# Kernel tuning notes

Hardware: AMD Instinct MI355X
Metric: run time of the kernel (lower is better)

## Reference

```python
import jax, jax.numpy as jnp
import numpy as np

N_NODES = 50000
N_EDGES = 800000
D = 64
IN_DIM = 100
N_GRAPHS = 512
N_LAYERS = 3
OUT_DIM = 24  # n_lbs * n_tasks
BN_EPS = 1e-5


def setup_inputs() -> dict:
    key = jax.random.key(0)
    ks = iter(jax.random.split(key, 40))

    def w(shape):
        fan_in = shape[0]
        return jax.random.normal(next(ks), shape, jnp.float32) / np.float32(np.sqrt(fan_in))

    inp = {}
    inp["x"] = jax.random.normal(next(ks), (N_NODES, IN_DIM), jnp.float32)
    inp["edge_index"] = jax.random.randint(next(ks), (2, N_EDGES), 0, N_NODES, jnp.int32)
    inp["batch"] = jnp.sort(jax.random.randint(next(ks), (N_NODES,), 0, N_GRAPHS, jnp.int32))

    dims_in = [IN_DIM, D, D]
    for i in range(N_LAYERS):
        inp[f"w1_{i}"] = w((dims_in[i], D))
        inp[f"b1_{i}"] = jnp.zeros((D,), jnp.float32)
        inp[f"w2_{i}"] = w((D, D))
        inp[f"b2_{i}"] = jnp.zeros((D,), jnp.float32)

    inp["jk_w"] = w((N_LAYERS * D, D))
    inp["jk_b"] = jnp.zeros((D,), jnp.float32)
    inp["ffn_w1"] = w((D, D))
    inp["ffn_b1"] = jnp.zeros((D,), jnp.float32)
    inp["bn_g"] = jnp.ones((D,), jnp.float32)
    inp["bn_b"] = jnp.zeros((D,), jnp.float32)
    inp["bn_m"] = 0.1 * jax.random.normal(next(ks), (D,), jnp.float32)
    inp["bn_v"] = jax.random.uniform(next(ks), (D,), jnp.float32, 0.5, 1.5)
    inp["ffn_w2"] = w((D, D))
    inp["ffn_b2"] = jnp.zeros((D,), jnp.float32)
    inp["out_w"] = w((D, OUT_DIM))
    inp["out_b"] = jnp.zeros((OUT_DIM,), jnp.float32)
    return inp


def _gin_conv(h, src, dst, w1, b1, w2, b2):
    # sum-aggregate neighbor messages:  agg[dst] += h[src]
    agg = jax.ops.segment_sum(h[src], dst, num_segments=N_NODES)
    z = h + agg  # eps = 0 -> (1 + eps) * x + agg
    # GINConv internal MLP: lin -> relu -> lin (no norm, plain last)
    return jnp.maximum(z @ w1 + b1, 0.0) @ w2 + b2


def reference(x, edge_index, batch,
              w1_0, b1_0, w2_0, b2_0,
              w1_1, b1_1, w2_1, b2_1,
              w1_2, b1_2, w2_2, b2_2,
              jk_w, jk_b,
              ffn_w1, ffn_b1, bn_g, bn_b, bn_m, bn_v, ffn_w2, ffn_b2,
              out_w, out_b):
    src, dst = edge_index[0], edge_index[1]
    layer_params = [(w1_0, b1_0, w2_0, b2_0),
                    (w1_1, b1_1, w2_1, b2_1),
                    (w1_2, b1_2, w2_2, b2_2)]
    xs = []
    h = x
    for (w1, b1, w2, b2) in layer_params:
        h = _gin_conv(h, src, dst, w1, b1, w2, b2)
        h = jnp.maximum(h, 0.0)  # inter-layer ReLU (jk='cat' applies it on every layer)
        xs.append(h)  # dropout is identity in eval
    # JumpingKnowledge 'cat' + final linear -> [N, D]
    h = jnp.concatenate(xs, axis=-1) @ jk_w + jk_b
    # global_add_pool -> [N_GRAPHS, D]
    g = jax.ops.segment_sum(h, batch, num_segments=N_GRAPHS)
    # ffn MLP: lin -> batchnorm (eval, running stats) -> relu -> lin
    t = g @ ffn_w1 + ffn_b1
    t = (t - bn_m) * jax.lax.rsqrt(bn_v + BN_EPS) * bn_g + bn_b
    t = jnp.maximum(t, 0.0) @ ffn_w2 + ffn_b2
    # output layer ('none' uncertainty): plain linear
    logits = t @ out_w + out_b
    return logits
```

## Files before the change

kernel.cpp:

```cpp
#include <hip/hip_runtime.h>

#define NN 50000
#define NE 800000
#define NG 512
#define INDIM 100
#define OUTD 24
#define LROW 72
#define XROW 136
#define NPART 8
#define PART_NODES 6250
#define CSR_CAP 64
#define B_WPREP 80
#define B_WPREP0 112
#define B_CNT0 308
#define B_GP0 692

typedef __attribute__((ext_vector_type(8))) short short8;
typedef __attribute__((ext_vector_type(4))) float floatx4;

__device__ inline float bf2f(unsigned short u) {
    unsigned v = (unsigned)u << 16;
    float f;
    __builtin_memcpy(&f, &v, 4);
    return f;
}
__device__ inline unsigned short f2bf(float f) {
    unsigned u;
    __builtin_memcpy(&u, &f, 4);
    u += 0x7fffu + ((u >> 16) & 1u);
    return (unsigned short)(u >> 16);
}


__global__ __launch_bounds__(256) void k_prep(const float* __restrict__ s0, const float* __restrict__ s1,
                                              const float* __restrict__ s2, const float* __restrict__ s3,
                                              const float* __restrict__ s4,
                                              const float* __restrict__ w1_0,
                                              unsigned short* __restrict__ wT,
                                              unsigned short* __restrict__ w0T,
                                              int* __restrict__ count,
                                              float* __restrict__ gp) {
    int b = blockIdx.x, tid = threadIdx.x;
    if (b < B_WPREP) {
        const float* srcs[5] = {s0, s1, s2, s3, s4};
        int id = b >> 4;
        int off = ((b & 15) << 8) + tid;
        int k = off >> 6, n = off & 63;
        wT[id * 4096 + n * 64 + k] = f2bf(srcs[id][k * 64 + n]);
    } else if (b < B_WPREP0) {
        int i = (b - B_WPREP) * 256 + tid;
        int n = i >> 7, k = i & 127;
        w0T[n * 128 + k] = (k < INDIM) ? f2bf(w1_0[k * 64 + n]) : 0;
    } else if (b < B_CNT0) {
        int i = (b - B_WPREP0) * 256 + tid;
        if (i < NN) count[i] = 0;
    } else {
        int i = (b - B_CNT0) * 256 + tid;
        if (i < 3 * NG * 64) gp[i] = 0.f;
    }
}


__global__ __launch_bounds__(256) void k_fill(const int* __restrict__ ei,
                                              int* __restrict__ count,
                                              int* __restrict__ csr) {
    int p = blockIdx.x & (NPART - 1);
    int slice = blockIdx.x >> 3;
    int nsl = gridDim.x >> 3;
    int lo = p * PART_NODES, hi = lo + PART_NODES;
    for (unsigned e = slice * 256u + threadIdx.x; e < NE; e += nsl * 256u) {
        int d = ei[NE + e];
        int s = ei[e];
        if (d >= lo && d < hi) {
            int pos = atomicAdd(&count[d], 1);
            if (pos < CSR_CAP) csr[(size_t)d * CSR_CAP + pos] = s;
        }
    }
}


__global__ __launch_bounds__(256) void k_pre0(const float* __restrict__ x,
                                              const unsigned short* __restrict__ w1T,
                                              unsigned short* __restrict__ y) {
    __shared__ __align__(16) unsigned short xs[64 * XROW];
    int tid = threadIdx.x;
    int base = blockIdx.x * 64;
    for (int i = tid; i < 64 * 128; i += 256) {
        int r = i >> 7, c = i & 127;
        int node = base + r;
        float v = (c < INDIM && node < NN) ? x[(size_t)node * INDIM + c] : 0.f;
        xs[r * XROW + c] = f2bf(v);
    }
    __syncthreads();
    int wave = tid >> 6, lane = tid & 63;
    int quad = lane >> 4, l15 = lane & 15;
#pragma unroll
    for (int nt = 0; nt < 4; ++nt) {
        floatx4 c = {0.f, 0.f, 0.f, 0.f};
#pragma unroll
        for (int kk = 0; kk < 4; ++kk) {
            short8 a = *(const short8*)&xs[(wave * 16 + l15) * XROW + kk * 32 + quad * 8];
            short8 bb = *(const short8*)&w1T[(nt * 16 + l15) * 128 + kk * 32 + quad * 8];
            c = __builtin_amdgcn_mfma_f32_16x16x32_bf16(a, bb, c, 0, 0, 0);
        }
        int col = nt * 16 + l15;
#pragma unroll
        for (int r = 0; r < 4; ++r) {
            int row = base + wave * 16 + quad * 4 + r;
            if (row < NN) y[(size_t)row * 64 + col] = f2bf(c[r]);
        }
    }
}


template <bool HAS_NEXT>
__global__ __launch_bounds__(256) void k_layer(const unsigned short* __restrict__ y,
                                               const int* __restrict__ count,
                                               const int* __restrict__ csr,
                                               const float* __restrict__ b1,
                                               const unsigned short* __restrict__ w2T,
                                               const float* __restrict__ b2,
                                               const unsigned short* __restrict__ wnT,
                                               unsigned short* __restrict__ ynext,
                                               const int* __restrict__ batch,
                                               float* __restrict__ gp) {
    __shared__ __align__(16) unsigned short tA[16 * LROW];
    __shared__ __align__(16) unsigned short tB[16 * LROW];
    int wave = threadIdx.x >> 6, lane = threadIdx.x & 63;
    int base = blockIdx.x * 16;
    float bias1 = b1[lane];

    for (int i = 0; i < 4; i += 2) {
        int nA = __builtin_amdgcn_readfirstlane(base + wave * 4 + i);
        int nB = __builtin_amdgcn_readfirstlane(base + wave * 4 + i + 1);
        int cA = min(count[nA], CSR_CAP);
        int cB = min(count[nB], CSR_CAP);
        const int* pA = csr + (size_t)nA * CSR_CAP;
        const int* pB = csr + (size_t)nB * CSR_CAP;
        float aA[4], aB[4];
        aA[0] = bf2f(y[(size_t)nA * 64 + lane]);
        aB[0] = bf2f(y[(size_t)nB * 64 + lane]);
        aA[1] = aA[2] = aA[3] = 0.f;
        aB[1] = aB[2] = aB[3] = 0.f;
        int eA = 0, eB = 0;
        while (eA + 8 <= cA && eB + 8 <= cB) {
            int iA[8], iB[8];
#pragma unroll
            for (int j = 0; j < 8; ++j) { iA[j] = pA[eA + j]; iB[j] = pB[eB + j]; }
            float vA[8], vB[8];
#pragma unroll
            for (int j = 0; j < 8; ++j) vA[j] = bf2f(y[(size_t)iA[j] * 64 + lane]);
#pragma unroll
            for (int j = 0; j < 8; ++j) vB[j] = bf2f(y[(size_t)iB[j] * 64 + lane]);
#pragma unroll
            for (int j = 0; j < 8; ++j) { aA[j & 3] += vA[j]; aB[j & 3] += vB[j]; }
            eA += 8; eB += 8;
        }
        for (; eA + 8 <= cA; eA += 8) {
            int idx[8];
#pragma unroll
            for (int j = 0; j < 8; ++j) idx[j] = pA[eA + j];
#pragma unroll
            for (int j = 0; j < 8; ++j) aA[j & 3] += bf2f(y[(size_t)idx[j] * 64 + lane]);
        }
        if (eA + 4 <= cA) {
            int i0 = pA[eA], i1 = pA[eA + 1], i2 = pA[eA + 2], i3 = pA[eA + 3];
            aA[0] += bf2f(y[(size_t)i0 * 64 + lane]);
            aA[1] += bf2f(y[(size_t)i1 * 64 + lane]);
            aA[2] += bf2f(y[(size_t)i2 * 64 + lane]);
            aA[3] += bf2f(y[(size_t)i3 * 64 + lane]);
            eA += 4;
        }
        if (eA + 2 <= cA) {
            int i0 = pA[eA], i1 = pA[eA + 1];
            aA[0] += bf2f(y[(size_t)i0 * 64 + lane]);
            aA[1] += bf2f(y[(size_t)i1 * 64 + lane]);
            eA += 2;
        }
        if (eA < cA) aA[0] += bf2f(y[(size_t)pA[eA] * 64 + lane]);
        for (; eB + 8 <= cB; eB += 8) {
            int idx[8];
#pragma unroll
            for (int j = 0; j < 8; ++j) idx[j] = pB[eB + j];
#pragma unroll
            for (int j = 0; j < 8; ++j) aB[j & 3] += bf2f(y[(size_t)idx[j] * 64 + lane]);
        }
        if (eB + 4 <= cB) {
            int i0 = pB[eB], i1 = pB[eB + 1], i2 = pB[eB + 2], i3 = pB[eB + 3];
            aB[0] += bf2f(y[(size_t)i0 * 64 + lane]);
            aB[1] += bf2f(y[(size_t)i1 * 64 + lane]);
            aB[2] += bf2f(y[(size_t)i2 * 64 + lane]);
            aB[3] += bf2f(y[(size_t)i3 * 64 + lane]);
            eB += 4;
        }
        if (eB + 2 <= cB) {
            int i0 = pB[eB], i1 = pB[eB + 1];
            aB[0] += bf2f(y[(size_t)i0 * 64 + lane]);
            aB[1] += bf2f(y[(size_t)i1 * 64 + lane]);
            eB += 2;
        }
        if (eB < cB) aB[0] += bf2f(y[(size_t)pB[eB] * 64 + lane]);

        float sA = (aA[0] + aA[1]) + (aA[2] + aA[3]);
        float sB = (aB[0] + aB[1]) + (aB[2] + aB[3]);
        tA[(wave * 4 + i) * LROW + lane]     = f2bf(fmaxf(sA + bias1, 0.f));
        tA[(wave * 4 + i + 1) * LROW + lane] = f2bf(fmaxf(sB + bias1, 0.f));
    }
    __syncthreads();

    int quad = lane >> 4, l15 = lane & 15;

    short8 a_k0 = *(const short8*)&tA[l15 * LROW + quad * 8];
    short8 a_k1 = *(const short8*)&tA[l15 * LROW + 32 + quad * 8];
    {
        int col = wave * 16 + l15;
        short8 b_k0 = *(const short8*)&w2T[col * 64 + quad * 8];
        short8 b_k1 = *(const short8*)&w2T[col * 64 + 32 + quad * 8];
        floatx4 c = {0.f, 0.f, 0.f, 0.f};
        c = __builtin_amdgcn_mfma_f32_16x16x32_bf16(a_k0, b_k0, c, 0, 0, 0);
        c = __builtin_amdgcn_mfma_f32_16x16x32_bf16(a_k1, b_k1, c, 0, 0, 0);
        float bb = b2[col];
#pragma unroll
        for (int r = 0; r < 4; ++r) {
            float h = fmaxf(c[r] + bb, 0.f);
            tB[(quad * 4 + r) * LROW + col] = f2bf(h);
        }
    }
    __syncthreads();

    if (wave == 0) {
        float run = 0.f;
        int curg = batch[base];
        for (int r = 0; r < 16; ++r) {
            int g2 = batch[base + r];
            if (g2 != curg) {
                atomicAdd(&gp[curg * 64 + lane], run);
                run = 0.f;
                curg = g2;
            }
            run += bf2f(tB[r * LROW + lane]);
        }
        atomicAdd(&gp[curg * 64 + lane], run);
    }

    if (HAS_NEXT) {
        short8 h_k0 = *(const short8*)&tB[l15 * LROW + quad * 8];
        short8 h_k1 = *(const short8*)&tB[l15 * LROW + 32 + quad * 8];
        int col = wave * 16 + l15;
        short8 w_k0 = *(const short8*)&wnT[col * 64 + quad * 8];
        short8 w_k1 = *(const short8*)&wnT[col * 64 + 32 + quad * 8];
        floatx4 cy = {0.f, 0.f, 0.f, 0.f};
        cy = __builtin_amdgcn_mfma_f32_16x16x32_bf16(h_k0, w_k0, cy, 0, 0, 0);
        cy = __builtin_amdgcn_mfma_f32_16x16x32_bf16(h_k1, w_k1, cy, 0, 0, 0);
#pragma unroll
        for (int r = 0; r < 4; ++r) {
            int row = base + quad * 4 + r;
            ynext[(size_t)row * 64 + col] = f2bf(cy[r]);
        }
    }
}


__device__ inline int lbound(const int* __restrict__ b, int v) {
    int lo = 0, hi = NN;
    while (lo < hi) {
        int m = (lo + hi) >> 1;
        if (b[m] < v) lo = m + 1; else hi = m;
    }
    return lo;
}

__global__ __launch_bounds__(64) void k_final(const float* __restrict__ gp,
                                              const int* __restrict__ batch,
                                              const float* __restrict__ jkw,
                                              const float* __restrict__ jkb,
                                              const float* __restrict__ w1,
                                              const float* __restrict__ b1,
                                              const float* __restrict__ bng,
                                              const float* __restrict__ bnb,
                                              const float* __restrict__ bnm,
                                              const float* __restrict__ bnv,
                                              const float* __restrict__ w2,
                                              const float* __restrict__ b2,
                                              const float* __restrict__ ow,
                                              const float* __restrict__ ob,
                                              float* __restrict__ out) {
    __shared__ float gs[192];
    __shared__ float gv[64];
    __shared__ float t2[64];
    __shared__ float t3[64];
    int gr = blockIdx.x, lane = threadIdx.x;
    gs[lane]       = gp[0 * NG * 64 + gr * 64 + lane];
    gs[64 + lane]  = gp[1 * NG * 64 + gr * 64 + lane];
    gs[128 + lane] = gp[2 * NG * 64 + gr * 64 + lane];
    float cntf = (float)(lbound(batch, gr + 1) - lbound(batch, gr));
    __syncthreads();
    float acc = cntf * jkb[lane];
#pragma unroll 8
    for (int k = 0; k < 192; ++k) acc = fmaf(gs[k], jkw[k * 64 + lane], acc);
    gv[lane] = acc;
    __syncthreads();
    acc = b1[lane];
#pragma unroll 8
    for (int k = 0; k < 64; ++k) acc = fmaf(gv[k], w1[k * 64 + lane], acc);
    acc = (acc - bnm[lane]) * rsqrtf(bnv[lane] + 1e-5f) * bng[lane] + bnb[lane];
    t2[lane] = fmaxf(acc, 0.f);
    __syncthreads();
    float acc2 = b2[lane];
#pragma unroll 8
    for (int k = 0; k < 64; ++k) acc2 = fmaf(t2[k], w2[k * 64 + lane], acc2);
    t3[lane] = acc2;
    __syncthreads();
    if (lane < OUTD) {
        float acc3 = ob[lane];
#pragma unroll 8
        for (int k = 0; k < 64; ++k) acc3 = fmaf(t3[k], ow[k * OUTD + lane], acc3);
        out[gr * OUTD + lane] = acc3;
    }
}

extern "C" void kernel_launch(void* const* d_in, const int* in_sizes, int n_in,
                              void* d_out, int out_size, void* d_ws, size_t ws_size,
                              hipStream_t stream) {
    const float* x     = (const float*)d_in[0];
    const int*   ei    = (const int*)d_in[1];
    const int*   batch = (const int*)d_in[2];
    const float* w1_0 = (const float*)d_in[3];
    const float* b1_0 = (const float*)d_in[4];
    const float* w2_0 = (const float*)d_in[5];
    const float* b2_0 = (const float*)d_in[6];
    const float* w1_1 = (const float*)d_in[7];
    const float* b1_1 = (const float*)d_in[8];
    const float* w2_1 = (const float*)d_in[9];
    const float* b2_1 = (const float*)d_in[10];
    const float* w1_2 = (const float*)d_in[11];
    const float* b1_2 = (const float*)d_in[12];
    const float* w2_2 = (const float*)d_in[13];
    const float* b2_2 = (const float*)d_in[14];
    const float* jk_w = (const float*)d_in[15];
    const float* jk_b = (const float*)d_in[16];
    const float* ffn_w1 = (const float*)d_in[17];
    const float* ffn_b1 = (const float*)d_in[18];
    const float* bn_g = (const float*)d_in[19];
    const float* bn_b = (const float*)d_in[20];
    const float* bn_m = (const float*)d_in[21];
    const float* bn_v = (const float*)d_in[22];
    const float* ffn_w2 = (const float*)d_in[23];
    const float* ffn_b2 = (const float*)d_in[24];
    const float* out_w  = (const float*)d_in[25];
    const float* out_b  = (const float*)d_in[26];

    float* ws = (float*)d_ws;
    unsigned short* ya = (unsigned short*)ws;
    unsigned short* yb = ya + 3200000;
    float* gp  = (float*)(yb + 3200000);
    int*   count = (int*)(gp + 3 * NG * 64);
    int*   csr   = count + NN;
    unsigned short* wT  = (unsigned short*)(csr + (size_t)NN * CSR_CAP);
    unsigned short* w0T = wT + 5 * 4096;

    k_prep<<<B_GP0, 256, 0, stream>>>(w2_0, w2_1, w2_2, w1_1, w1_2, w1_0,
                                      wT, w0T, count, gp);

    k_fill<<<NPART * 192, 256, 0, stream>>>(ei, count, csr);
    k_pre0<<<(NN + 63) / 64, 256, 0, stream>>>(x, w0T, ya);

    int nblk = NN / 16;
    k_layer<true><<<nblk, 256, 0, stream>>>(ya, count, csr, b1_0,
                                            wT + 0 * 4096, b2_0, wT + 3 * 4096,
                                            yb, batch, gp + 0 * NG * 64);
    k_layer<true><<<nblk, 256, 0, stream>>>(yb, count, csr, b1_1,
                                            wT + 1 * 4096, b2_1, wT + 4 * 4096,
                                            ya, batch, gp + 1 * NG * 64);
    k_layer<false><<<nblk, 256, 0, stream>>>(ya, count, csr, b1_2,
                                             wT + 2 * 4096, b2_2, nullptr,
                                             nullptr, batch, gp + 2 * NG * 64);

    k_final<<<NG, 64, 0, stream>>>(gp, batch, jk_w, jk_b,
                                   ffn_w1, ffn_b1, bn_g, bn_b, bn_m, bn_v,
                                   ffn_w2, ffn_b2, out_w, out_b, (float*)d_out);
}
```

Before: 263.8 us.

## Vectorize neighbor gather with 16-byte row loads and merge fill with pre0 kernel

The gather in each layer kernel now has each lane load 8 bf16 features (16 bytes) from one neighbor, with 8 lanes per row and 8 neighbors per wave step. Partial sums are combined with cross-lane shuffles, and a zero padding row at index NN replaces the tail branches. This is meant to cut the number of gather memory instructions and the per-edge loop overhead, at the cost of shuffle reductions and wasted lanes on low-degree nodes. The CSR fill and the first-layer projection kernels are also merged into one launch so the two independent jobs can overlap.

```diff
diff --git a/kernel.cpp b/kernel.cpp
--- a/kernel.cpp
+++ b/kernel.cpp
@@ -10,13 +10,17 @@
 #define NPART 8
 #define PART_NODES 6250
 #define CSR_CAP 64
+#define YSZ 3200512
 #define B_WPREP 80
 #define B_WPREP0 112
 #define B_CNT0 308
 #define B_GP0 692
+#define FBLK 1536
+#define PBLK 782
 
 typedef __attribute__((ext_vector_type(8))) short short8;
 typedef __attribute__((ext_vector_type(4))) float floatx4;
+typedef __attribute__((ext_vector_type(4))) unsigned int uintx4;
 
 __device__ inline float bf2f(unsigned short u) {
     unsigned v = (unsigned)u << 16;
@@ -29,6 +33,24 @@
     __builtin_memcpy(&u, &f, 4);
     u += 0x7fffu + ((u >> 16) & 1u);
     return (unsigned short)(u >> 16);
+}
+
+__device__ inline void acc8(float* a, uintx4 v) {
+#pragma unroll
+    for (int j = 0; j < 4; ++j) {
+        unsigned u = v[j];
+        unsigned lo = u << 16;
+        unsigned hi = u & 0xffff0000u;
+        float flo, fhi;
+        __builtin_memcpy(&flo, &lo, 4);
+        __builtin_memcpy(&fhi, &hi, 4);
+        a[2 * j]     += flo;
+        a[2 * j + 1] += fhi;
+    }
+}
+
+__device__ inline uintx4 ldrow(const unsigned short* __restrict__ y, int idx, int sub) {
+    return *(const uintx4*)&y[(size_t)idx * 64 + sub * 8];
 }
 
 
@@ -39,7 +61,9 @@
                                               unsigned short* __restrict__ wT,
                                               unsigned short* __restrict__ w0T,
                                               int* __restrict__ count,
-                                              float* __restrict__ gp) {
+                                              float* __restrict__ gp,
+                                              unsigned short* __restrict__ ya,
+                                              unsigned short* __restrict__ yb) {
     int b = blockIdx.x, tid = threadIdx.x;
     if (b < B_WPREP) {
         const float* srcs[5] = {s0, s1, s2, s3, s4};
@@ -54,6 +78,10 @@
     } else if (b < B_CNT0) {
         int i = (b - B_WPREP0) * 256 + tid;
         if (i < NN) count[i] = 0;
+        if (i < 64) {
+            ya[(size_t)NN * 64 + i] = 0;
+            yb[(size_t)NN * 64 + i] = 0;
+        }
     } else {
         int i = (b - B_CNT0) * 256 + tid;
         if (i < 3 * NG * 64) gp[i] = 0.f;
@@ -61,30 +89,30 @@
 }
 
 
-__global__ __launch_bounds__(256) void k_fill(const int* __restrict__ ei,
-                                              int* __restrict__ count,
-                                              int* __restrict__ csr) {
-    int p = blockIdx.x & (NPART - 1);
-    int slice = blockIdx.x >> 3;
-    int nsl = gridDim.x >> 3;
-    int lo = p * PART_NODES, hi = lo + PART_NODES;
-    for (unsigned e = slice * 256u + threadIdx.x; e < NE; e += nsl * 256u) {
-        int d = ei[NE + e];
-        int s = ei[e];
-        if (d >= lo && d < hi) {
-            int pos = atomicAdd(&count[d], 1);
-            if (pos < CSR_CAP) csr[(size_t)d * CSR_CAP + pos] = s;
-        }
-    }
-}
-
-
-__global__ __launch_bounds__(256) void k_pre0(const float* __restrict__ x,
-                                              const unsigned short* __restrict__ w1T,
-                                              unsigned short* __restrict__ y) {
+__global__ __launch_bounds__(256) void k_mid(const int* __restrict__ ei,
+                                             int* __restrict__ count,
+                                             int* __restrict__ csr,
+                                             const float* __restrict__ x,
+                                             const unsigned short* __restrict__ w1T,
+                                             unsigned short* __restrict__ y) {
     __shared__ __align__(16) unsigned short xs[64 * XROW];
     int tid = threadIdx.x;
-    int base = blockIdx.x * 64;
+    if (blockIdx.x < FBLK) {
+        int p = blockIdx.x & (NPART - 1);
+        int slice = blockIdx.x >> 3;
+        int nsl = FBLK >> 3;
+        int lo = p * PART_NODES, hi = lo + PART_NODES;
+        for (unsigned e = slice * 256u + tid; e < NE; e += nsl * 256u) {
+            int d = ei[NE + e];
+            int s = ei[e];
+            if (d >= lo && d < hi) {
+                int pos = atomicAdd(&count[d], 1);
+                if (pos < CSR_CAP) csr[(size_t)d * CSR_CAP + pos] = s;
+            }
+        }
+        return;
+    }
+    int base = (blockIdx.x - FBLK) * 64;
     for (int i = tid; i < 64 * 128; i += 256) {
         int r = i >> 7, c = i & 127;
         int node = base + r;
@@ -127,8 +155,13 @@
     __shared__ __align__(16) unsigned short tA[16 * LROW];
     __shared__ __align__(16) unsigned short tB[16 * LROW];
     int wave = threadIdx.x >> 6, lane = threadIdx.x & 63;
+    int slot = lane >> 3;
+    int sub  = lane & 7;
     int base = blockIdx.x * 16;
-    float bias1 = b1[lane];
+
+    float bias1v[8];
+    *(floatx4*)&bias1v[0] = *(const floatx4*)&b1[sub * 8];
+    *(floatx4*)&bias1v[4] = *(const floatx4*)&b1[sub * 8 + 4];
 
     for (int i = 0; i < 4; i += 2) {
         int nA = __builtin_amdgcn_readfirstlane(base + wave * 4 + i);
@@ -137,74 +170,60 @@
         int cB = min(count[nB], CSR_CAP);
         const int* pA = csr + (size_t)nA * CSR_CAP;
         const int* pB = csr + (size_t)nB * CSR_CAP;
-        float aA[4], aB[4];
-        aA[0] = bf2f(y[(size_t)nA * 64 + lane]);
-        aB[0] = bf2f(y[(size_t)nB * 64 + lane]);
-        aA[1] = aA[2] = aA[3] = 0.f;
-        aB[1] = aB[2] = aB[3] = 0.f;
-        int eA = 0, eB = 0;
-        while (eA + 8 <= cA && eB + 8 <= cB) {
-            int iA[8], iB[8];
-#pragma unroll
-            for (int j = 0; j < 8; ++j) { iA[j] = pA[eA + j]; iB[j] = pB[eB + j]; }
-            float vA[8], vB[8];
-#pragma unroll
-            for (int j = 0; j < 8; ++j) vA[j] = bf2f(y[(size_t)iA[j] * 64 + lane]);
-#pragma unroll
-            for (int j = 0; j < 8; ++j) vB[j] = bf2f(y[(size_t)iB[j] * 64 + lane]);
-#pragma unroll
-            for (int j = 0; j < 8; ++j) { aA[j & 3] += vA[j]; aB[j & 3] += vB[j]; }
-            eA += 8; eB += 8;
-        }
-        for (; eA + 8 <= cA; eA += 8) {
-            int idx[8];
-#pragma unroll
-            for (int j = 0; j < 8; ++j) idx[j] = pA[eA + j];
-#pragma unroll
-            for (int j = 0; j < 8; ++j) aA[j & 3] += bf2f(y[(size_t)idx[j] * 64 + lane]);
-        }
-        if (eA + 4 <= cA) {
-            int i0 = pA[eA], i1 = pA[eA + 1], i2 = pA[eA + 2], i3 = pA[eA + 3];
-            aA[0] += bf2f(y[(size_t)i0 * 64 + lane]);
-            aA[1] += bf2f(y[(size_t)i1 * 64 + lane]);
-            aA[2] += bf2f(y[(size_t)i2 * 64 + lane]);
-            aA[3] += bf2f(y[(size_t)i3 * 64 + lane]);
-            eA += 4;
-        }
-        if (eA + 2 <= cA) {
-            int i0 = pA[eA], i1 = pA[eA + 1];
-            aA[0] += bf2f(y[(size_t)i0 * 64 + lane]);
-            aA[1] += bf2f(y[(size_t)i1 * 64 + lane]);
-            eA += 2;
-        }
-        if (eA < cA) aA[0] += bf2f(y[(size_t)pA[eA] * 64 + lane]);
-        for (; eB + 8 <= cB; eB += 8) {
-            int idx[8];
-#pragma unroll
-            for (int j = 0; j < 8; ++j) idx[j] = pB[eB + j];
-#pragma unroll
-            for (int j = 0; j < 8; ++j) aB[j & 3] += bf2f(y[(size_t)idx[j] * 64 + lane]);
-        }
-        if (eB + 4 <= cB) {
-            int i0 = pB[eB], i1 = pB[eB + 1], i2 = pB[eB + 2], i3 = pB[eB + 3];
-            aB[0] += bf2f(y[(size_t)i0 * 64 + lane]);
-            aB[1] += bf2f(y[(size_t)i1 * 64 + lane]);
-            aB[2] += bf2f(y[(size_t)i2 * 64 + lane]);
-            aB[3] += bf2f(y[(size_t)i3 * 64 + lane]);
-            eB += 4;
-        }
-        if (eB + 2 <= cB) {
-            int i0 = pB[eB], i1 = pB[eB + 1];
-            aB[0] += bf2f(y[(size_t)i0 * 64 + lane]);
-            aB[1] += bf2f(y[(size_t)i1 * 64 + lane]);
-            eB += 2;
-        }
-        if (eB < cB) aB[0] += bf2f(y[(size_t)pB[eB] * 64 + lane]);
-
-        float sA = (aA[0] + aA[1]) + (aA[2] + aA[3]);
-        float sB = (aB[0] + aB[1]) + (aB[2] + aB[3]);
-        tA[(wave * 4 + i) * LROW + lane]     = f2bf(fmaxf(sA + bias1, 0.f));
-        tA[(wave * 4 + i + 1) * LROW + lane] = f2bf(fmaxf(sB + bias1, 0.f));
+        float accA[8], accB[8];
+#pragma unroll
+        for (int j = 0; j < 8; ++j) { accA[j] = 0.f; accB[j] = 0.f; }
+
+        int ia0 = (slot < cA)     ? pA[slot]     : NN;
+        int ia1 = (8 + slot < cA) ? pA[8 + slot] : NN;
+        int ib0 = (slot < cB)     ? pB[slot]     : NN;
+        int ib1 = (8 + slot < cB) ? pB[8 + slot] : NN;
+        uintx4 va0 = ldrow(y, ia0, sub);
+        uintx4 vb0 = ldrow(y, ib0, sub);
+        uintx4 va1 = ldrow(y, ia1, sub);
+        uintx4 vb1 = ldrow(y, ib1, sub);
+        acc8(accA, va0); acc8(accA, va1);
+        acc8(accB, vb0); acc8(accB, vb1);
+
+        int npA = (cA + 7) >> 3, npB = (cB + 7) >> 3;
+        int np = max(npA, npB);
+        for (int t = 2; t < np; ++t) {
+            int e = t * 8 + slot;
+            if (t < npA) {
+                int ia = (e < cA) ? pA[e] : NN;
+                acc8(accA, ldrow(y, ia, sub));
+            }
+            if (t < npB) {
+                int ib = (e < cB) ? pB[e] : NN;
+                acc8(accB, ldrow(y, ib, sub));
+            }
+        }
+
+#pragma unroll
+        for (int j = 0; j < 8; ++j) {
+            accA[j] += __shfl_xor(accA[j], 8);
+            accA[j] += __shfl_xor(accA[j], 16);
+            accA[j] += __shfl_xor(accA[j], 32);
+            accB[j] += __shfl_xor(accB[j], 8);
+            accB[j] += __shfl_xor(accB[j], 16);
+            accB[j] += __shfl_xor(accB[j], 32);
+        }
+
+        uintx4 svA = ldrow(y, nA, sub);
+        uintx4 svB = ldrow(y, nB, sub);
+        acc8(accA, svA);
+        acc8(accB, svB);
+
+        short8 oA, oB;
+#pragma unroll
+        for (int j = 0; j < 8; ++j) {
+            oA[j] = (short)f2bf(fmaxf(accA[j] + bias1v[j], 0.f));
+            oB[j] = (short)f2bf(fmaxf(accB[j] + bias1v[j], 0.f));
+        }
+        if (slot == 0) {
+            *(short8*)&tA[(wave * 4 + i) * LROW + sub * 8]     = oA;
+            *(short8*)&tA[(wave * 4 + i + 1) * LROW + sub * 8] = oB;
+        }
     }
     __syncthreads();
 
@@ -352,18 +371,17 @@
 
     float* ws = (float*)d_ws;
     unsigned short* ya = (unsigned short*)ws;
-    unsigned short* yb = ya + 3200000;
-    float* gp  = (float*)(yb + 3200000);
+    unsigned short* yb = ya + YSZ;
+    float* gp  = (float*)(yb + YSZ);
     int*   count = (int*)(gp + 3 * NG * 64);
     int*   csr   = count + NN;
     unsigned short* wT  = (unsigned short*)(csr + (size_t)NN * CSR_CAP);
     unsigned short* w0T = wT + 5 * 4096;
 
     k_prep<<<B_GP0, 256, 0, stream>>>(w2_0, w2_1, w2_2, w1_1, w1_2, w1_0,
-                                      wT, w0T, count, gp);
-
-    k_fill<<<NPART * 192, 256, 0, stream>>>(ei, count, csr);
-    k_pre0<<<(NN + 63) / 64, 256, 0, stream>>>(x, w0T, ya);
+                                      wT, w0T, count, gp, ya, yb);
+
+    k_mid<<<FBLK + PBLK, 256, 0, stream>>>(ei, count, csr, x, w0T, ya);
 
     int nblk = NN / 16;
     k_layer<true><<<nblk, 256, 0, stream>>>(ya, count, csr, b1_0,
```

Result: slower. 279.1 us (+5.8%).
